# Kernel optimization log

Measured on AMD Instinct MI355X. Metric: run time of the kernel, lower is better.

Reference implementation:

```python
import jax, jax.numpy as jnp
import numpy as np

NBINS = 51
BIN_WIDTH = 2.0 / (NBINS - 1)
BS, D = 1024, 128
N_CLASSES = 32


def setup_inputs() -> dict:
    key = jax.random.key(0)
    kx, kl = jax.random.split(key)
    x = jax.random.normal(kx, (BS, D), dtype=jnp.float32)
    x = x / jnp.linalg.norm(x, axis=1, keepdims=True)  # similarities in [-1, 1]
    labels = jax.random.randint(kl, (BS,), 0, N_CLASSES, dtype=jnp.int64)
    return {"x": x, "labels": labels}


def reference(x, labels):
    # Pairwise similarities of upper-triangular (i < j) pairs.
    sim = x @ x.T                                   # [bs, bs]
    bs = x.shape[0]
    iu, ju = jnp.triu_indices(bs, k=1)              # n_pairs indices
    s = sim[iu, ju]                                 # [n_pairs]
    pos = labels[iu] == labels[ju]                  # [n_pairs] bool

    # Soft (linear) binning: pair with sim s assigned bin value v = floor((s+1)/bw)*bw - 1
    # contributes (v+bw-s)/bw to bin b and (s-v)/bw to bin b+1 (triangular kernel),
    # exactly matching the original indsa/indsb masking scheme.
    b = jnp.floor((s + 1.0) / BIN_WIDTH).astype(jnp.int32)  # bin index in [0, nbins-1]
    v = b.astype(s.dtype) * BIN_WIDTH - 1.0                  # assigned bin value
    w_lo = (v + BIN_WIDTH - s) / BIN_WIDTH                   # weight for bin b
    w_hi = (s - v) / BIN_WIDTH                               # weight for bin b+1
    b_hi = jnp.clip(b + 1, 0, NBINS - 1)                     # w_hi == 0 when clipped

    def hist(mask):
        m = mask.astype(s.dtype)
        h = jnp.zeros((NBINS,), s.dtype)
        h = h.at[b].add(w_lo * m)
        h = h.at[b_hi].add(w_hi * m)
        return h / m.sum()

    hist_pos = hist(pos)
    hist_neg = hist(~pos)

    # CDF of positive histogram, then histogram loss.
    hist_pos_cdf = jnp.cumsum(hist_pos)
    return jnp.sum(hist_neg * hist_pos_cdf)
```

## Files before the change

kernel.cpp:

```cpp
#include <hip/hip_runtime.h>

#define NBINS 51
#define NT    32
#define TILE  32
#define DV4   32

__global__ __launch_bounds__(256) void pair_hist_kernel(
    const float* __restrict__ x,
    const int*   __restrict__ labels,
    float*       __restrict__ ghist)
{
    __shared__ float4 As[TILE][DV4];
    __shared__ float4 Bs[TILE][DV4];
    __shared__ int    la[TILE], lb[TILE];
    __shared__ float  shist[2 * NBINS];

    int rem = blockIdx.x;
    int bi = 0;
    while (rem >= NT - bi) { rem -= NT - bi; ++bi; }
    const int bj = bi + rem;

    const float4* xv = (const float4*)x;
    const int t = threadIdx.x;

    #pragma unroll
    for (int k = 0; k < 4; ++k) {
        int e = t + 256 * k;
        int r = e >> 5;
        int c = e & 31;
        int sw = c ^ ((r >> 1) & 7);
        As[r][sw] = xv[(bi * TILE + r) * DV4 + c];
        Bs[r][sw] = xv[(bj * TILE + r) * DV4 + c];
    }
    if (t < TILE) {
        la[t] = labels[bi * TILE + t];
        lb[t] = labels[bj * TILE + t];
    }
    if (t < 2 * NBINS) shist[t] = 0.0f;
    __syncthreads();

    const int tx = t & 15;
    const int ty = t >> 4;
    const int i0 = ty * 2, j0 = tx * 2;
    const int kA = ty & 7;
    const int kB = tx & 7;

    float acc00 = 0.f, acc01 = 0.f, acc10 = 0.f, acc11 = 0.f;
    #pragma unroll
    for (int d4 = 0; d4 < DV4; ++d4) {
        float4 a0 = As[i0    ][d4 ^ kA];
        float4 a1 = As[i0 + 1][d4 ^ kA];
        float4 b0 = Bs[j0    ][d4 ^ kB];
        float4 b1 = Bs[j0 + 1][d4 ^ kB];
        acc00 += a0.x*b0.x + a0.y*b0.y + a0.z*b0.z + a0.w*b0.w;
        acc01 += a0.x*b1.x + a0.y*b1.y + a0.z*b1.z + a0.w*b1.w;
        acc10 += a1.x*b0.x + a1.y*b0.y + a1.z*b0.z + a1.w*b0.w;
        acc11 += a1.x*b1.x + a1.y*b1.y + a1.z*b1.z + a1.w*b1.w;
    }

    const float BW = 2.0f / (NBINS - 1);
    float accs[2][2] = {{acc00, acc01}, {acc10, acc11}};

    #pragma unroll
    for (int r = 0; r < 2; ++r) {
        #pragma unroll
        for (int c = 0; c < 2; ++c) {
            int gi = bi * TILE + i0 + r;
            int gj = bj * TILE + j0 + c;
            if (gi < gj) {
                float s = accs[r][c];
                int b = (int)floorf((s + 1.0f) / BW);
                b = min(max(b, 0), NBINS - 1);
                float v = (float)b * BW - 1.0f;
                float wlo = (v + BW - s) / BW;
                float whi = (s - v) / BW;
                int bh = min(b + 1, NBINS - 1);
                int base = (la[i0 + r] == lb[j0 + c]) ? 0 : NBINS;
                atomicAdd(&shist[base + b],  wlo);
                atomicAdd(&shist[base + bh], whi);
            }
        }
    }

    __syncthreads();
    if (t < 2 * NBINS) atomicAdd(&ghist[t], shist[t]);
}

__global__ void finalize_kernel(const float* __restrict__ gh,
                                float* __restrict__ out)
{
    int t = threadIdx.x;
    float hp = (t < NBINS) ? gh[t]         : 0.0f;
    float hn = (t < NBINS) ? gh[NBINS + t] : 0.0f;

    float sp = hp, sn = hn;
    #pragma unroll
    for (int off = 32; off > 0; off >>= 1) {
        sp += __shfl_xor(sp, off, 64);
        sn += __shfl_xor(sn, off, 64);
    }

    float cdf = hp;
    #pragma unroll
    for (int off = 1; off < 64; off <<= 1) {
        float v = __shfl_up(cdf, off, 64);
        if (t >= off) cdf += v;
    }

    float contrib = hn * cdf;
    #pragma unroll
    for (int off = 32; off > 0; off >>= 1)
        contrib += __shfl_xor(contrib, off, 64);

    if (t == 0) out[0] = contrib / (sp * sn);
}

extern "C" void kernel_launch(void* const* d_in, const int* in_sizes, int n_in,
                              void* d_out, int out_size, void* d_ws, size_t ws_size,
                              hipStream_t stream)
{
    const float* x      = (const float*)d_in[0];
    const int*   labels = (const int*)d_in[1];
    float*       ghist  = (float*)d_ws;

    hipMemsetAsync(ghist, 0, 2 * NBINS * sizeof(float), stream);
    pair_hist_kernel<<<NT * (NT + 1) / 2, 256, 0, stream>>>(x, labels, ghist);
    finalize_kernel<<<1, 64, 0, stream>>>(ghist, (float*)d_out);
}
```

Before: 84.99 us.

## Privatize shared histograms and replace global atomics with per-block partials

```diff
diff --git a/kernel.cpp b/kernel.cpp
--- a/kernel.cpp
+++ b/kernel.cpp
@@ -4,25 +4,29 @@
 #define NT    32
 #define TILE  32
 #define DV4   32
+#define NBLK  (NT * (NT + 1) / 2)
+#define NCOPY 16
+#define HSTR  103
 
 __global__ __launch_bounds__(256) void pair_hist_kernel(
     const float* __restrict__ x,
     const int*   __restrict__ labels,
-    float*       __restrict__ ghist)
+    float*       __restrict__ partial)
 {
     __shared__ float4 As[TILE][DV4];
     __shared__ float4 Bs[TILE][DV4];
     __shared__ int    la[TILE], lb[TILE];
-    __shared__ float  shist[2 * NBINS];
+    __shared__ float  shist[NCOPY * HSTR];
 
     int rem = blockIdx.x;
     int bi = 0;
     while (rem >= NT - bi) { rem -= NT - bi; ++bi; }
     const int bj = bi + rem;
 
+    const int t = threadIdx.x;
+    for (int k = t; k < NCOPY * HSTR; k += 256) shist[k] = 0.0f;
+
     const float4* xv = (const float4*)x;
-    const int t = threadIdx.x;
-
     #pragma unroll
     for (int k = 0; k < 4; ++k) {
         int e = t + 256 * k;
@@ -36,7 +40,6 @@
         la[t] = labels[bi * TILE + t];
         lb[t] = labels[bj * TILE + t];
     }
-    if (t < 2 * NBINS) shist[t] = 0.0f;
     __syncthreads();
 
     const int tx = t & 15;
@@ -46,7 +49,7 @@
     const int kB = tx & 7;
 
     float acc00 = 0.f, acc01 = 0.f, acc10 = 0.f, acc11 = 0.f;
-    #pragma unroll
+    #pragma unroll 4
     for (int d4 = 0; d4 < DV4; ++d4) {
         float4 a0 = As[i0    ][d4 ^ kA];
         float4 a1 = As[i0 + 1][d4 ^ kA];
@@ -60,6 +63,7 @@
 
     const float BW = 2.0f / (NBINS - 1);
     float accs[2][2] = {{acc00, acc01}, {acc10, acc11}};
+    float* myh = &shist[(t & (NCOPY - 1)) * HSTR];
 
     #pragma unroll
     for (int r = 0; r < 2; ++r) {
@@ -76,54 +80,75 @@
                 float whi = (s - v) / BW;
                 int bh = min(b + 1, NBINS - 1);
                 int base = (la[i0 + r] == lb[j0 + c]) ? 0 : NBINS;
-                atomicAdd(&shist[base + b],  wlo);
-                atomicAdd(&shist[base + bh], whi);
+                atomicAdd(&myh[base + b],  wlo);
+                atomicAdd(&myh[base + bh], whi);
             }
         }
     }
 
     __syncthreads();
-    if (t < 2 * NBINS) atomicAdd(&ghist[t], shist[t]);
+    if (t < 2 * NBINS) {
+        float s = 0.f;
+        #pragma unroll
+        for (int c = 0; c < NCOPY; ++c) s += shist[c * HSTR + t];
+        partial[t * NBLK + blockIdx.x] = s;
+    }
 }
 
-__global__ void finalize_kernel(const float* __restrict__ gh,
-                                float* __restrict__ out)
+__global__ __launch_bounds__(1024) void finalize_kernel(
+    const float* __restrict__ partial,
+    float*       __restrict__ out)
 {
-    int t = threadIdx.x;
-    float hp = (t < NBINS) ? gh[t]         : 0.0f;
-    float hn = (t < NBINS) ? gh[NBINS + t] : 0.0f;
+    __shared__ float h[2 * NBINS];
+    const int t = threadIdx.x;
+    const int wave = t >> 6, lane = t & 63;
 
-    float sp = hp, sn = hn;
-    #pragma unroll
-    for (int off = 32; off > 0; off >>= 1) {
-        sp += __shfl_xor(sp, off, 64);
-        sn += __shfl_xor(sn, off, 64);
+    for (int bin = wave; bin < 2 * NBINS; bin += 16) {
+        float s = 0.f;
+        for (int idx = lane; idx < NBLK; idx += 64)
+            s += partial[bin * NBLK + idx];
+        #pragma unroll
+        for (int off = 32; off > 0; off >>= 1)
+            s += __shfl_xor(s, off, 64);
+        if (lane == 0) h[bin] = s;
     }
+    __syncthreads();
 
-    float cdf = hp;
-    #pragma unroll
-    for (int off = 1; off < 64; off <<= 1) {
-        float v = __shfl_up(cdf, off, 64);
-        if (t >= off) cdf += v;
+    if (t < 64) {
+        float hp = (t < NBINS) ? h[t]         : 0.0f;
+        float hn = (t < NBINS) ? h[NBINS + t] : 0.0f;
+
+        float sp = hp, sn = hn;
+        #pragma unroll
+        for (int off = 32; off > 0; off >>= 1) {
+            sp += __shfl_xor(sp, off, 64);
+            sn += __shfl_xor(sn, off, 64);
+        }
+
+        float cdf = hp;
+        #pragma unroll
+        for (int off = 1; off < 64; off <<= 1) {
+            float v = __shfl_up(cdf, off, 64);
+            if (t >= off) cdf += v;
+        }
+
+        float contrib = hn * cdf;
+        #pragma unroll
+        for (int off = 32; off > 0; off >>= 1)
+            contrib += __shfl_xor(contrib, off, 64);
+
+        if (t == 0) out[0] = contrib / (sp * sn);
     }
-
-    float contrib = hn * cdf;
-    #pragma unroll
-    for (int off = 32; off > 0; off >>= 1)
-        contrib += __shfl_xor(contrib, off, 64);
-
-    if (t == 0) out[0] = contrib / (sp * sn);
 }
 
 extern "C" void kernel_launch(void* const* d_in, const int* in_sizes, int n_in,
                               void* d_out, int out_size, void* d_ws, size_t ws_size,
                               hipStream_t stream)
 {
-    const float* x      = (const float*)d_in[0];
-    const int*   labels = (const int*)d_in[1];
-    float*       ghist  = (float*)d_ws;
+    const float* x       = (const float*)d_in[0];
+    const int*   labels  = (const int*)d_in[1];
+    float*       partial = (float*)d_ws;
 
-    hipMemsetAsync(ghist, 0, 2 * NBINS * sizeof(float), stream);
-    pair_hist_kernel<<<NT * (NT + 1) / 2, 256, 0, stream>>>(x, labels, ghist);
-    finalize_kernel<<<1, 64, 0, stream>>>(ghist, (float*)d_out);
+    pair_hist_kernel<<<NBLK, 256, 0, stream>>>(x, labels, partial);
+    finalize_kernel<<<1, 1024, 0, stream>>>(partial, (float*)d_out);
 }
```

New measurement: 89.83 us. +5.7%, slower.
